# Kernel optimization log

Hardware: AMD Instinct MI355X
Metric: run time of the kernel (lower is better)

Reference implementation:

```python
import jax, jax.numpy as jnp
import numpy as np
from jax import lax

B, C, H, W = 4, 256, 64, 64
C8 = C // 8  # 32


def setup_inputs() -> dict:
    key = jax.random.key(0)
    ks = jax.random.split(key, 8)
    x = jax.random.normal(ks[0], (B, C, H, W), jnp.float32)
    # 1x1 conv weights stored as [out_ch, in_ch]
    wb = jax.random.normal(ks[1], (C8, 2 * C), jnp.float32) * 0.02
    bb = jax.random.normal(ks[2], (C8,), jnp.float32) * 0.02
    wc = jax.random.normal(ks[3], (C8, 2 * C), jnp.float32) * 0.02
    bc = jax.random.normal(ks[4], (C8,), jnp.float32) * 0.02
    wd = jax.random.normal(ks[5], (C, 2 * C), jnp.float32) * 0.02
    bd = jax.random.normal(ks[6], (C,), jnp.float32) * 0.02
    alpha = jnp.float32(0.5)  # nn.Parameter(zeros(1)) at init; nonzero for a meaningful test
    return {"x": x, "wb": wb, "bb": bb, "wc": wc, "bc": bc, "wd": wd, "bd": bd, "alpha": alpha}


def reference(x, wb, bb, wc, bc, wd, bd, alpha):
    b, c, h, w = x.shape
    n = h * w
    pad = [(0, 0), (0, 0), (1, 1), (1, 1)]
    # F.avg_pool2d(k=3, s=1, p=1) with count_include_pad=True -> window-sum / 9
    x_avg = lax.reduce_window(x, 0.0, lax.add, (1, 1, 3, 3), (1, 1, 1, 1), pad) / 9.0
    x_max = lax.reduce_window(x, -jnp.inf, lax.max, (1, 1, 3, 3), (1, 1, 1, 1), pad)
    cat = jnp.concatenate([x_avg, x_max], axis=1)  # [B, 2C, H, W]
    catf = cat.reshape(b, 2 * c, n)                # [B, 2C, N]
    # 1x1 convs == per-pixel linear projections
    feat_b = jnp.einsum('oc,bcn->bon', wb, catf) + bb[None, :, None]  # [B, C8, N]
    feat_c = jnp.einsum('oc,bcn->bon', wc, catf) + bc[None, :, None]  # [B, C8, N]
    feat_d = jnp.einsum('oc,bcn->bon', wd, catf) + bd[None, :, None]  # [B, C,  N]
    # attention_s = softmax(feat_b^T @ feat_c) over last dim -> [B, N, N]
    attn = jax.nn.softmax(jnp.einsum('bon,bom->bnm', feat_b, feat_c), axis=-1)
    # feat_e = feat_d @ attn^T -> [B, C, N]
    feat_e = jnp.einsum('bcn,bmn->bcm', feat_d, attn).reshape(b, c, h, w)
    return alpha * feat_e + (1.0 - alpha) * x
```

## Files before the change

### kernel.cpp

```cpp
#include <hip/hip_runtime.h>
#include <hip/hip_bf16.h>

typedef __hip_bfloat16 bf16;
typedef __attribute__((ext_vector_type(8))) short s8v;
typedef __attribute__((ext_vector_type(4))) float f4v;

__device__ __forceinline__ ushort f2u(float f) {
    bf16 h = __float2bfloat16(f);
    return *(ushort*)&h;
}


__global__ __launch_bounds__(256) void wcvt_kernel(
    const float* __restrict__ wb, const float* __restrict__ wc,
    const float* __restrict__ wd, ushort* __restrict__ Wf) {
    int f = blockIdx.x * 4 + (threadIdx.x >> 6);
    int l = threadIdx.x & 63;
    int ot = f % 20, kc = f / 20;
    int o = ot * 16 + (l & 15);
    int k0 = kc * 32 + (l >> 4) * 8;
    const float* wr = (o < 32) ? wb + (size_t)o * 512
                    : (o < 64) ? wc + (size_t)(o - 32) * 512
                               : wd + (size_t)(o - 64) * 512;
    float4 f0 = *(const float4*)(wr + k0);
    float4 f1 = *(const float4*)(wr + k0 + 4);
    ushort tmp[8] = {f2u(f0.x), f2u(f0.y), f2u(f0.z), f2u(f0.w),
                     f2u(f1.x), f2u(f1.y), f2u(f1.z), f2u(f1.w)};
    *(uint4*)(Wf + kc * 10240 + ot * 512 + l * 8) = *(uint4*)tmp;
}

__global__ __launch_bounds__(512, 2) void fused_kernel(
    const float* __restrict__ x, const ushort* __restrict__ Wf,
    const float* __restrict__ bb, const float* __restrict__ bc,
    const float* __restrict__ bd,
    ushort* __restrict__ Qb, ushort* __restrict__ Kb, ushort* __restrict__ Vf) {
    __shared__ __align__(16) char smem[117248];
    float*  Xs   = (float*)smem;
    ushort* Vls  = (ushort*)smem;
    ushort* catS = (ushort*)(smem + 50688);

    int tid = threadIdx.x;
    int bid = blockIdx.x;
    int lb = (bid & 7) * 32 + (bid >> 3);
    int b = lb >> 6, h = lb & 63;
    bool hasU = (h > 0), hasD = (h < 63);

    float4 xr[6];
#define LOADCG(CG)                                                              \
    {                                                                           \
        _Pragma("unroll")                                                       \
        for (int pp = 0; pp < 6; ++pp) {                                        \
            int linear = pp * 512 + tid;                                        \
            int w4 = linear & 15, cs_s = (linear >> 4) & 63, dh = linear >> 10; \
            int hh = h + dh - 1;                                                \
            float4 fv = {0.f, 0.f, 0.f, 0.f};                                   \
            if ((unsigned)hh < 64u)                                             \
                fv = *(const float4*)(x + ((size_t)(b * 256 + (CG) * 64 + cs_s)) * 4096 \
                                      + hh * 64 + w4 * 4);                      \
            xr[pp] = fv;                                                        \
        }                                                                       \
    }
    LOADCG(0)
    #pragma unroll
    for (int cg = 0; cg < 4; ++cg) {
        #pragma unroll
        for (int pp = 0; pp < 6; ++pp) {
            int linear = pp * 512 + tid;
            int w4 = linear & 15, cs_s = (linear >> 4) & 63, dh = linear >> 10;
            float* xp = Xs + (dh * 64 + w4 * 4) * 66 + cs_s;
            xp[0]   = xr[pp].x;
            xp[66]  = xr[pp].y;
            xp[132] = xr[pp].z;
            xp[198] = xr[pp].w;
        }
        __syncthreads();
        if (cg == 0) LOADCG(1)
        else if (cg == 1) LOADCG(2)
        else if (cg == 2) LOADCG(3)
        {
            int cs = tid & 63, wsw = tid >> 6;
            float vs[10], vm[10];
            #pragma unroll
            for (int j = 0; j < 10; ++j) {
                int w = wsw * 8 - 1 + j;
                if ((unsigned)w < 64u) {
                    float u = Xs[w * 66 + cs];
                    float m = Xs[(64 + w) * 66 + cs];
                    float d = Xs[(128 + w) * 66 + cs];
                    vs[j] = u + m + d;
                    float mx = m;
                    if (hasU) mx = fmaxf(mx, u);
                    if (hasD) mx = fmaxf(mx, d);
                    vm[j] = mx;
                } else { vs[j] = 0.f; vm[j] = -3.4e38f; }
            }
            int chb = cg * 64 + cs;
            #pragma unroll
            for (int i = 0; i < 8; ++i) {
                float sum = vs[i] + vs[i + 1] + vs[i + 2];
                float mx  = fmaxf(fmaxf(vm[i], vm[i + 1]), vm[i + 2]);
                catS[(wsw * 8 + i) * 520 + chb]       = f2u(sum * (1.f / 9.f));
                catS[(wsw * 8 + i) * 520 + 256 + chb] = f2u(mx);
            }
        }
        __syncthreads();
    }
#undef LOADCG

    int l = tid & 63, w = tid >> 6;
    int lm = l & 15, q = l >> 4;
    int nc = w & 3, oh = w >> 2;
    f4v pacc[10];
    #pragma unroll
    for (int ot = 0; ot < 10; ++ot)
        #pragma unroll
        for (int i = 0; i < 4; ++i) pacc[ot][i] = 0.f;

    const ushort* wfp = Wf + (oh * 10) * 512 + l * 8;
    const ushort* ap  = catS + (nc * 16 + lm) * 520 + q * 8;
    #pragma unroll 2
    for (int kci = 0; kci < 16; ++kci) {
        s8v Af = *(const s8v*)(ap + kci * 32);
        s8v Bf[10];
        #pragma unroll
        for (int ot = 0; ot < 10; ++ot)
            Bf[ot] = *(const s8v*)(wfp + kci * 10240 + ot * 512);
        #pragma unroll
        for (int ot = 0; ot < 10; ++ot)
            pacc[ot] = __builtin_amdgcn_mfma_f32_16x16x32_bf16(Af, Bf[ot], pacc[ot], 0, 0, 0);
    }

    size_t nrow = (size_t)((b << 12) + h * 64 + nc * 16 + q * 4);
    if (oh == 0) {
        #pragma unroll
        for (int ot = 0; ot < 2; ++ot) {
            int o = ot * 16 + lm;
            float bias = bb[o];
            #pragma unroll
            for (int r = 0; r < 4; ++r)
                Qb[(nrow + r) * 32 + o] = f2u(pacc[ot][r] + bias);
        }
        #pragma unroll
        for (int ot = 2; ot < 4; ++ot) {
            int o = ot * 16 + lm - 32;
            float bias = bc[o];
            #pragma unroll
            for (int r = 0; r < 4; ++r)
                Kb[(nrow + r) * 32 + o] = f2u(pacc[ot][r] + bias);
        }
        #pragma unroll
        for (int ot = 4; ot < 10; ++ot) {
            int c = ot * 16 + lm - 64;
            float bias = bd[c];
            ushort tmp[4];
            #pragma unroll
            for (int r = 0; r < 4; ++r) tmp[r] = f2u(pacc[ot][r] + bias);
            *(uint2*)&Vls[c * 72 + nc * 16 + q * 4] = *(uint2*)tmp;
        }
    } else {
        #pragma unroll
        for (int ot = 0; ot < 10; ++ot) {
            int c = 96 + ot * 16 + lm;
            float bias = bd[c];
            ushort tmp[4];
            #pragma unroll
            for (int r = 0; r < 4; ++r) tmp[r] = f2u(pacc[ot][r] + bias);
            *(uint2*)&Vls[c * 72 + nc * 16 + q * 4] = *(uint2*)tmp;
        }
    }
    __syncthreads();
    {
        size_t vb = ((size_t)b << 20) + (size_t)(h * 2) * 8192 + l * 8;
        #pragma unroll
        for (int i = 0; i < 2; ++i) {
            int cb = w * 2 + i;
            #pragma unroll
            for (int nh = 0; nh < 2; ++nh)
                *(uint4*)(Vf + vb + nh * 8192 + cb * 512)
                    = *(const uint4*)&Vls[(cb * 16 + lm) * 72 + nh * 32 + q * 8];
        }
    }
}

__global__ __launch_bounds__(512, 2) void attn_kernel(
    const ushort* __restrict__ Qb, const ushort* __restrict__ Kb,
    const ushort* __restrict__ Vf, const float* __restrict__ x,
    const float* __restrict__ alphap, float* __restrict__ out) {
    __shared__ __align__(16) ushort Ps[2][64][72];
    __shared__ float Obuf[4][64][17];
    __shared__ float Lpart[4][64];
    __shared__ float Lrow[64];
    int tid = threadIdx.x;
    int l = tid & 63, w = tid >> 6;
    int lm = l & 15, q = l >> 4;
    int nsw = w & 3, kh = w >> 2;
    int bid = blockIdx.x;
    int xcd = bid & 7;
    int b = xcd & 3;
    int midx = (bid >> 3) + ((xcd >> 2) << 5);
    int m0 = midx << 6;
    size_t bN = (size_t)b << 12;

    s8v Qf[2];
    {
        const ushort* qb = Qb + (bN + m0 + kh * 32) * 32;
        Qf[0] = *(const s8v*)(qb + (size_t)(lm) * 32 + q * 8);
        Qf[1] = *(const s8v*)(qb + (size_t)(16 + lm) * 32 + q * 8);
    }
    const ushort* kbp = Kb + (bN + nsw * 16 + lm) * 32 + q * 8;
    const ushort* vfp = Vf + ((size_t)b << 20) + kh * 8192 + (nsw * 4) * 512 + l * 8;

    f4v acc[4][4];
    #pragma unroll
    for (int mt = 0; mt < 4; ++mt)
        #pragma unroll
        for (int ct = 0; ct < 4; ++ct)
            #pragma unroll
            for (int i = 0; i < 4; ++i) acc[mt][ct][i] = 0.f;
    float La0 = 0.f, La1 = 0.f;

    s8v kf0 = *(const s8v*)kbp;
    s8v kf1 = *(const s8v*)(kbp + 2048);
    s8v vfA[4], vfB[4];
    #pragma unroll
    for (int ct = 0; ct < 4; ++ct) vfA[ct] = *(const s8v*)(vfp + ct * 512);
    {
        f4v S0 = {0.f, 0.f, 0.f, 0.f}, S1 = {0.f, 0.f, 0.f, 0.f};
        S0 = __builtin_amdgcn_mfma_f32_16x16x32_bf16(kf0, Qf[0], S0, 0, 0, 0);
        S1 = __builtin_amdgcn_mfma_f32_16x16x32_bf16(kf0, Qf[1], S1, 0, 0, 0);
        ushort e0[4], e1[4];
        #pragma unroll
        for (int r = 0; r < 4; ++r) {
            float f0 = __expf(fminf(S0[r], 60.f));
            float f1 = __expf(fminf(S1[r], 60.f));
            La0 += f0; La1 += f1;
            e0[r] = f2u(f0); e1[r] = f2u(f1);
        }
        *(uint2*)&Ps[0][kh * 32 + lm][nsw * 16 + q * 4]      = *(uint2*)e0;
        *(uint2*)&Ps[0][kh * 32 + 16 + lm][nsw * 16 + q * 4] = *(uint2*)e1;
    }
    __syncthreads();

#define TILE_BODY(TT, KFS, KFP, VCUR, VNXT)                                       \
    {                                                                             \
        int p = (TT) & 1;                                                         \
        if ((TT) < 62) KFP = *(const s8v*)(kbp + (size_t)((TT) + 2) * 2048);      \
        if ((TT) < 63) {                                                          \
            const ushort* vn = vfp + (size_t)((TT) + 1) * 16384;                  \
            _Pragma("unroll")                                                     \
            for (int ct = 0; ct < 4; ++ct)                                        \
                VNXT[ct] = *(const s8v*)(vn + ct * 512);                          \
        }                                                                         \
        f4v S0 = {0.f, 0.f, 0.f, 0.f}, S1 = {0.f, 0.f, 0.f, 0.f};                 \
        if ((TT) < 63) {                                                          \
            S0 = __builtin_amdgcn_mfma_f32_16x16x32_bf16(KFS, Qf[0], S0, 0, 0, 0);\
            S1 = __builtin_amdgcn_mfma_f32_16x16x32_bf16(KFS, Qf[1], S1, 0, 0, 0);\
        }                                                                         \
        s8v Af0 = *(const s8v*)&Ps[p][lm][kh * 32 + q * 8];                       \
        s8v Af1 = *(const s8v*)&Ps[p][16 + lm][kh * 32 + q * 8];                  \
        s8v Af2 = *(const s8v*)&Ps[p][32 + lm][kh * 32 + q * 8];                  \
        s8v Af3 = *(const s8v*)&Ps[p][48 + lm][kh * 32 + q * 8];                  \
        if ((TT) < 63) {                                                          \
            ushort e0[4], e1[4];                                                  \
            _Pragma("unroll")                                                     \
            for (int r = 0; r < 4; ++r) {                                         \
                float f0 = __expf(fminf(S0[r], 60.f));                            \
                float f1 = __expf(fminf(S1[r], 60.f));                            \
                La0 += f0; La1 += f1;                                             \
                e0[r] = f2u(f0); e1[r] = f2u(f1);                                 \
            }                                                                     \
            *(uint2*)&Ps[1 - p][kh * 32 + lm][nsw * 16 + q * 4]      = *(uint2*)e0;\
            *(uint2*)&Ps[1 - p][kh * 32 + 16 + lm][nsw * 16 + q * 4] = *(uint2*)e1;\
        }                                                                         \
        _Pragma("unroll")                                                         \
        for (int ct = 0; ct < 4; ++ct) {                                          \
            acc[0][ct] = __builtin_amdgcn_mfma_f32_16x16x32_bf16(Af0, VCUR[ct], acc[0][ct], 0, 0, 0); \
            acc[1][ct] = __builtin_amdgcn_mfma_f32_16x16x32_bf16(Af1, VCUR[ct], acc[1][ct], 0, 0, 0); \
            acc[2][ct] = __builtin_amdgcn_mfma_f32_16x16x32_bf16(Af2, VCUR[ct], acc[2][ct], 0, 0, 0); \
            acc[3][ct] = __builtin_amdgcn_mfma_f32_16x16x32_bf16(Af3, VCUR[ct], acc[3][ct], 0, 0, 0); \
        }                                                                         \
        asm volatile("s_waitcnt lgkmcnt(0)\n\ts_barrier" ::: "memory");           \
    }

    for (int t = 0; t < 64; t += 2) {
        TILE_BODY(t,     kf1, kf0, vfA, vfB);
        TILE_BODY(t + 1, kf0, kf1, vfB, vfA);
    }
#undef TILE_BODY

    La0 += __shfl_xor(La0, 16, 64); La0 += __shfl_xor(La0, 32, 64);
    La1 += __shfl_xor(La1, 16, 64); La1 += __shfl_xor(La1, 32, 64);
    if (q == 0) {
        Lpart[nsw][kh * 32 + lm]      = La0;
        Lpart[nsw][kh * 32 + 16 + lm] = La1;
    }
    __syncthreads();
    if (tid < 64)
        Lrow[tid] = Lpart[0][tid] + Lpart[1][tid] + Lpart[2][tid] + Lpart[3][tid];
    __syncthreads();
    #pragma unroll
    for (int ct = 0; ct < 4; ++ct) {
        if (kh == 1) {
            #pragma unroll
            for (int mt = 0; mt < 4; ++mt)
                #pragma unroll
                for (int r = 0; r < 4; ++r)
                    Obuf[nsw][mt * 16 + q * 4 + r][lm] = acc[mt][ct][r];
        }
        __syncthreads();
        if (kh == 0) {
            #pragma unroll
            for (int mt = 0; mt < 4; ++mt)
                #pragma unroll
                for (int r = 0; r < 4; ++r)
                    acc[mt][ct][r] += Obuf[nsw][mt * 16 + q * 4 + r][lm];
        }
        __syncthreads();
    }
    if (kh == 0) {
        float alpha = alphap[0];
        float ra = 1.f - alpha;
        #pragma unroll
        for (int mt = 0; mt < 4; ++mt) {
            float L0 = Lrow[mt * 16 + q * 4 + 0];
            float L1 = Lrow[mt * 16 + q * 4 + 1];
            float L2 = Lrow[mt * 16 + q * 4 + 2];
            float L3 = Lrow[mt * 16 + q * 4 + 3];
            #pragma unroll
            for (int ct = 0; ct < 4; ++ct) {
                int cc = nsw * 64 + ct * 16 + lm;
                size_t base = ((size_t)(b * 256 + cc)) * 4096 + m0 + mt * 16 + q * 4;
                float4 xv = *(const float4*)(x + base);
                float4 ov;
                ov.x = alpha * (acc[mt][ct][0] / L0) + ra * xv.x;
                ov.y = alpha * (acc[mt][ct][1] / L1) + ra * xv.y;
                ov.z = alpha * (acc[mt][ct][2] / L2) + ra * xv.z;
                ov.w = alpha * (acc[mt][ct][3] / L3) + ra * xv.w;
                *(float4*)(out + base) = ov;
            }
        }
    }
}

extern "C" void kernel_launch(void* const* d_in, const int* in_sizes, int n_in,
                              void* d_out, int out_size, void* d_ws, size_t ws_size,
                              hipStream_t stream) {
    const float* x  = (const float*)d_in[0];
    const float* wb = (const float*)d_in[1];
    const float* bb = (const float*)d_in[2];
    const float* wc = (const float*)d_in[3];
    const float* bc = (const float*)d_in[4];
    const float* wd = (const float*)d_in[5];
    const float* bd = (const float*)d_in[6];
    const float* al = (const float*)d_in[7];
    float* out = (float*)d_out;

    char* ws = (char*)d_ws;
    ushort* Qb = (ushort*)ws;
    ushort* Kb = (ushort*)(ws + 1048576);
    ushort* Vf = (ushort*)(ws + 2097152);
    ushort* Wf = (ushort*)(ws + 10485760);

    wcvt_kernel<<<dim3(80), dim3(256), 0, stream>>>(wb, wc, wd, Wf);
    fused_kernel<<<dim3(256), dim3(512), 0, stream>>>(x, Wf, bb, bc, bd,
                                                      Qb, Kb, Vf);
    attn_kernel<<<dim3(256), dim3(512), 0, stream>>>(Qb, Kb, Vf, x, al, out);
}
```

Before: 164.2 us.

## Specialize warps into score producers and PV consumers with wider key tiles

Splits the 8 waves of the attention block into 4 producer waves that compute QK^T scores and exponentials into shared memory, and 4 consumer waves that run the P·V MFMAs. Key tiles grow from 64 to 128 per phase, so the loop runs 32 phases instead of 64 and needs half as many barriers. Because the consumer waves each own the full K range for their channels, the cross-half reduction through shared memory at the end goes away. The trade-offs are unbalanced work between the two wave groups, more registers per consumer wave (16 V fragments), and a larger shared P buffer.

```diff
diff --git a/kernel.cpp b/kernel.cpp
--- a/kernel.cpp
+++ b/kernel.cpp
@@ -186,14 +186,12 @@
     const ushort* __restrict__ Qb, const ushort* __restrict__ Kb,
     const ushort* __restrict__ Vf, const float* __restrict__ x,
     const float* __restrict__ alphap, float* __restrict__ out) {
-    __shared__ __align__(16) ushort Ps[2][64][72];
-    __shared__ float Obuf[4][64][17];
+    __shared__ __align__(16) ushort Ps[2][64][132];
     __shared__ float Lpart[4][64];
     __shared__ float Lrow[64];
     int tid = threadIdx.x;
     int l = tid & 63, w = tid >> 6;
     int lm = l & 15, q = l >> 4;
-    int nsw = w & 3, kh = w >> 2;
     int bid = blockIdx.x;
     int xcd = bid & 7;
     int b = xcd & 3;
@@ -201,123 +199,131 @@
     int m0 = midx << 6;
     size_t bN = (size_t)b << 12;
 
-    s8v Qf[2];
-    {
-        const ushort* qb = Qb + (bN + m0 + kh * 32) * 32;
-        Qf[0] = *(const s8v*)(qb + (size_t)(lm) * 32 + q * 8);
-        Qf[1] = *(const s8v*)(qb + (size_t)(16 + lm) * 32 + q * 8);
-    }
-    const ushort* kbp = Kb + (bN + nsw * 16 + lm) * 32 + q * 8;
-    const ushort* vfp = Vf + ((size_t)b << 20) + kh * 8192 + (nsw * 4) * 512 + l * 8;
-
+    bool isS = (w < 4);
+    int nsw = w & 3;
+
+    s8v Qf[4];
+    s8v kfA[2], kfB[2];
+    float La[4] = {0.f, 0.f, 0.f, 0.f};
     f4v acc[4][4];
-    #pragma unroll
-    for (int mt = 0; mt < 4; ++mt)
-        #pragma unroll
-        for (int ct = 0; ct < 4; ++ct)
-            #pragma unroll
-            for (int i = 0; i < 4; ++i) acc[mt][ct][i] = 0.f;
-    float La0 = 0.f, La1 = 0.f;
-
-    s8v kf0 = *(const s8v*)kbp;
-    s8v kf1 = *(const s8v*)(kbp + 2048);
-    s8v vfA[4], vfB[4];
-    #pragma unroll
-    for (int ct = 0; ct < 4; ++ct) vfA[ct] = *(const s8v*)(vfp + ct * 512);
-    {
-        f4v S0 = {0.f, 0.f, 0.f, 0.f}, S1 = {0.f, 0.f, 0.f, 0.f};
-        S0 = __builtin_amdgcn_mfma_f32_16x16x32_bf16(kf0, Qf[0], S0, 0, 0, 0);
-        S1 = __builtin_amdgcn_mfma_f32_16x16x32_bf16(kf0, Qf[1], S1, 0, 0, 0);
-        ushort e0[4], e1[4];
-        #pragma unroll
-        for (int r = 0; r < 4; ++r) {
-            float f0 = __expf(fminf(S0[r], 60.f));
-            float f1 = __expf(fminf(S1[r], 60.f));
-            La0 += f0; La1 += f1;
-            e0[r] = f2u(f0); e1[r] = f2u(f1);
-        }
-        *(uint2*)&Ps[0][kh * 32 + lm][nsw * 16 + q * 4]      = *(uint2*)e0;
-        *(uint2*)&Ps[0][kh * 32 + 16 + lm][nsw * 16 + q * 4] = *(uint2*)e1;
+    s8v vf[16];
+
+    const ushort* kbp = Kb + (bN + nsw * 32 + lm) * 32 + q * 8;
+    const ushort* vfp = Vf + ((size_t)b << 20) + (nsw * 4) * 512 + l * 8;
+
+    if (isS) {
+        #pragma unroll
+        for (int h = 0; h < 4; ++h)
+            Qf[h] = *(const s8v*)(Qb + (bN + m0 + h * 16 + lm) * 32 + q * 8);
+        s8v k00 = *(const s8v*)(kbp);
+        s8v k01 = *(const s8v*)(kbp + 512);
+        kfB[0] = *(const s8v*)(kbp + 4096);
+        kfB[1] = *(const s8v*)(kbp + 4096 + 512);
+        #pragma unroll
+        for (int c = 0; c < 2; ++c) {
+            s8v kc = c ? k01 : k00;
+            #pragma unroll
+            for (int h = 0; h < 4; ++h) {
+                f4v S = {0.f, 0.f, 0.f, 0.f};
+                S = __builtin_amdgcn_mfma_f32_16x16x32_bf16(kc, Qf[h], S, 0, 0, 0);
+                ushort e[4];
+                #pragma unroll
+                for (int r = 0; r < 4; ++r) {
+                    float f = __expf(fminf(S[r], 60.f));
+                    La[h] += f; e[r] = f2u(f);
+                }
+                *(uint2*)&Ps[0][h * 16 + lm][nsw * 32 + c * 16 + q * 4] = *(uint2*)e;
+            }
+        }
+    } else {
+        #pragma unroll
+        for (int mt = 0; mt < 4; ++mt)
+            #pragma unroll
+            for (int ct = 0; ct < 4; ++ct)
+                #pragma unroll
+                for (int i = 0; i < 4; ++i) acc[mt][ct][i] = 0.f;
+        #pragma unroll
+        for (int i = 0; i < 16; ++i)
+            vf[i] = *(const s8v*)(vfp + (i >> 2) * 8192 + (i & 3) * 512);
     }
     __syncthreads();
 
-#define TILE_BODY(TT, KFS, KFP, VCUR, VNXT)                                       \
+#define PHASE(TT, KFS, KFP)                                                       \
     {                                                                             \
         int p = (TT) & 1;                                                         \
-        if ((TT) < 62) KFP = *(const s8v*)(kbp + (size_t)((TT) + 2) * 2048);      \
-        if ((TT) < 63) {                                                          \
-            const ushort* vn = vfp + (size_t)((TT) + 1) * 16384;                  \
+        if (isS) {                                                                \
+            if ((TT) < 30) {                                                      \
+                const ushort* kn = kbp + (size_t)((TT) + 2) * 4096;               \
+                KFP[0] = *(const s8v*)kn;                                         \
+                KFP[1] = *(const s8v*)(kn + 512);                                 \
+            }                                                                     \
+            if ((TT) < 31) {                                                      \
+                _Pragma("unroll")                                                 \
+                for (int c = 0; c < 2; ++c) {                                     \
+                    _Pragma("unroll")                                             \
+                    for (int h = 0; h < 4; ++h) {                                 \
+                        f4v S = {0.f, 0.f, 0.f, 0.f};                             \
+                        S = __builtin_amdgcn_mfma_f32_16x16x32_bf16(              \
+                                KFS[c], Qf[h], S, 0, 0, 0);                       \
+                        ushort e[4];                                              \
+                        _Pragma("unroll")                                         \
+                        for (int r = 0; r < 4; ++r) {                             \
+                            float f = __expf(fminf(S[r], 60.f));                  \
+                            La[h] += f; e[r] = f2u(f);                            \
+                        }                                                         \
+                        *(uint2*)&Ps[1 - p][h * 16 + lm][nsw * 32 + c * 16 + q * 4] \
+                            = *(uint2*)e;                                         \
+                    }                                                             \
+                }                                                                 \
+            }                                                                     \
+        } else {                                                                  \
+            const ushort* vn = vfp + (size_t)((TT) + 1) * 32768;                  \
             _Pragma("unroll")                                                     \
-            for (int ct = 0; ct < 4; ++ct)                                        \
-                VNXT[ct] = *(const s8v*)(vn + ct * 512);                          \
-        }                                                                         \
-        f4v S0 = {0.f, 0.f, 0.f, 0.f}, S1 = {0.f, 0.f, 0.f, 0.f};                 \
-        if ((TT) < 63) {                                                          \
-            S0 = __builtin_amdgcn_mfma_f32_16x16x32_bf16(KFS, Qf[0], S0, 0, 0, 0);\
-            S1 = __builtin_amdgcn_mfma_f32_16x16x32_bf16(KFS, Qf[1], S1, 0, 0, 0);\
-        }                                                                         \
-        s8v Af0 = *(const s8v*)&Ps[p][lm][kh * 32 + q * 8];                       \
-        s8v Af1 = *(const s8v*)&Ps[p][16 + lm][kh * 32 + q * 8];                  \
-        s8v Af2 = *(const s8v*)&Ps[p][32 + lm][kh * 32 + q * 8];                  \
-        s8v Af3 = *(const s8v*)&Ps[p][48 + lm][kh * 32 + q * 8];                  \
-        if ((TT) < 63) {                                                          \
-            ushort e0[4], e1[4];                                                  \
-            _Pragma("unroll")                                                     \
-            for (int r = 0; r < 4; ++r) {                                         \
-                float f0 = __expf(fminf(S0[r], 60.f));                            \
-                float f1 = __expf(fminf(S1[r], 60.f));                            \
-                La0 += f0; La1 += f1;                                             \
-                e0[r] = f2u(f0); e1[r] = f2u(f1);                                 \
+            for (int ks = 0; ks < 4; ++ks) {                                      \
+                s8v Af[4];                                                        \
+                _Pragma("unroll")                                                 \
+                for (int mt = 0; mt < 4; ++mt)                                    \
+                    Af[mt] = *(const s8v*)&Ps[p][mt * 16 + lm][ks * 32 + q * 8];  \
+                _Pragma("unroll")                                                 \
+                for (int ct = 0; ct < 4; ++ct) {                                  \
+                    _Pragma("unroll")                                             \
+                    for (int mt = 0; mt < 4; ++mt)                                \
+                        acc[mt][ct] = __builtin_amdgcn_mfma_f32_16x16x32_bf16(    \
+                            Af[mt], vf[ks * 4 + ct], acc[mt][ct], 0, 0, 0);       \
+                }                                                                 \
+                if ((TT) < 31) {                                                  \
+                    _Pragma("unroll")                                             \
+                    for (int ct = 0; ct < 4; ++ct)                                \
+                        vf[ks * 4 + ct] = *(const s8v*)(vn + ks * 8192 + ct * 512); \
+                }                                                                 \
             }                                                                     \
-            *(uint2*)&Ps[1 - p][kh * 32 + lm][nsw * 16 + q * 4]      = *(uint2*)e0;\
-            *(uint2*)&Ps[1 - p][kh * 32 + 16 + lm][nsw * 16 + q * 4] = *(uint2*)e1;\
-        }                                                                         \
-        _Pragma("unroll")                                                         \
-        for (int ct = 0; ct < 4; ++ct) {                                          \
-            acc[0][ct] = __builtin_amdgcn_mfma_f32_16x16x32_bf16(Af0, VCUR[ct], acc[0][ct], 0, 0, 0); \
-            acc[1][ct] = __builtin_amdgcn_mfma_f32_16x16x32_bf16(Af1, VCUR[ct], acc[1][ct], 0, 0, 0); \
-            acc[2][ct] = __builtin_amdgcn_mfma_f32_16x16x32_bf16(Af2, VCUR[ct], acc[2][ct], 0, 0, 0); \
-            acc[3][ct] = __builtin_amdgcn_mfma_f32_16x16x32_bf16(Af3, VCUR[ct], acc[3][ct], 0, 0, 0); \
         }                                                                         \
         asm volatile("s_waitcnt lgkmcnt(0)\n\ts_barrier" ::: "memory");           \
     }
 
-    for (int t = 0; t < 64; t += 2) {
-        TILE_BODY(t,     kf1, kf0, vfA, vfB);
-        TILE_BODY(t + 1, kf0, kf1, vfB, vfA);
-    }
-#undef TILE_BODY
-
-    La0 += __shfl_xor(La0, 16, 64); La0 += __shfl_xor(La0, 32, 64);
-    La1 += __shfl_xor(La1, 16, 64); La1 += __shfl_xor(La1, 32, 64);
-    if (q == 0) {
-        Lpart[nsw][kh * 32 + lm]      = La0;
-        Lpart[nsw][kh * 32 + 16 + lm] = La1;
+    for (int t = 0; t < 32; t += 2) {
+        PHASE(t,     kfB, kfA);
+        PHASE(t + 1, kfA, kfB);
+    }
+#undef PHASE
+
+    if (isS) {
+        #pragma unroll
+        for (int h = 0; h < 4; ++h) {
+            La[h] += __shfl_xor(La[h], 16, 64);
+            La[h] += __shfl_xor(La[h], 32, 64);
+        }
+        if (q == 0) {
+            #pragma unroll
+            for (int h = 0; h < 4; ++h)
+                Lpart[nsw][h * 16 + lm] = La[h];
+        }
     }
     __syncthreads();
     if (tid < 64)
         Lrow[tid] = Lpart[0][tid] + Lpart[1][tid] + Lpart[2][tid] + Lpart[3][tid];
     __syncthreads();
-    #pragma unroll
-    for (int ct = 0; ct < 4; ++ct) {
-        if (kh == 1) {
-            #pragma unroll
-            for (int mt = 0; mt < 4; ++mt)
-                #pragma unroll
-                for (int r = 0; r < 4; ++r)
-                    Obuf[nsw][mt * 16 + q * 4 + r][lm] = acc[mt][ct][r];
-        }
-        __syncthreads();
-        if (kh == 0) {
-            #pragma unroll
-            for (int mt = 0; mt < 4; ++mt)
-                #pragma unroll
-                for (int r = 0; r < 4; ++r)
-                    acc[mt][ct][r] += Obuf[nsw][mt * 16 + q * 4 + r][lm];
-        }
-        __syncthreads();
-    }
-    if (kh == 0) {
+    if (!isS) {
         float alpha = alphap[0];
         float ra = 1.f - alpha;
         #pragma unroll
```

Measured after the change: 155.2 us. -5.5%, faster.
